# Performance work log

Hardware: AMD Instinct MI355X
Metric: run time of the kernel (lower is better)

## Reference

```python
import jax, jax.numpy as jnp
import numpy as np

N_NODES = 50000
E = 800000
D = 64
H = 128


def _ln(x, g, b, eps=1e-5):
    m = x.mean(-1, keepdims=True)
    v = ((x - m) ** 2).mean(-1, keepdims=True)
    return (x - m) * jax.lax.rsqrt(v + eps) * g + b


def setup_inputs() -> dict:
    key = jax.random.key(0)
    ks = jax.random.split(key, 8)
    return dict(
        node_emb=jax.random.normal(ks[0], (N_NODES, D), jnp.float32),
        src=jax.random.randint(ks[1], (E,), 0, N_NODES),
        dst=jax.random.randint(ks[2], (E,), 0, N_NODES),
        noise=jax.random.uniform(ks[3], (E,), jnp.float32, 1e-6, 1.0 - 1e-6),
        W1=jax.random.normal(ks[4], (2 * D, H), jnp.float32) * 0.05,
        b1=jnp.zeros((H,), jnp.float32),
        g1=jnp.ones((H,), jnp.float32),
        bt1=jnp.zeros((H,), jnp.float32),
        W2=jax.random.normal(ks[5], (H, H // 2), jnp.float32) * 0.05,
        b2=jnp.zeros((H // 2,), jnp.float32),
        g2=jnp.ones((H // 2,), jnp.float32),
        bt2=jnp.zeros((H // 2,), jnp.float32),
        W3=jax.random.normal(ks[6], (H // 2, 1), jnp.float32) * 0.05,
        b3=jnp.zeros((1,), jnp.float32),
    )


def reference(node_emb, src, dst, noise, W1, b1, g1, bt1, W2, b2, g2, bt2, W3, b3):
    # edge gather + concat: [E, 2D]
    edge_emb = jnp.concatenate([node_emb[src], node_emb[dst]], axis=1)
    # edge MLP with LayerNorm + relu (dropout=0 / eval)
    h = jax.nn.relu(_ln(edge_emb @ W1 + b1, g1, bt1))
    h = jax.nn.relu(_ln(h @ W2 + b2, g2, bt2))
    logit = (h @ W3 + b3).reshape(-1)  # [E]
    # concrete gate, bias=0, beta=1.0 (forward default)
    beta = 1.0
    gate = jax.nn.sigmoid((jnp.log(noise) - jnp.log1p(-noise) + logit) / beta)
    # degree norm: out_deg(src)^-1/2 * in_deg(dst)^-1/2, degrees clamped to >=1
    ones = jnp.ones((src.shape[0],), node_emb.dtype)
    out_deg = jnp.maximum(jax.ops.segment_sum(ones, src, num_segments=N_NODES), 1.0)
    in_deg = jnp.maximum(jax.ops.segment_sum(ones, dst, num_segments=N_NODES), 1.0)
    norm = jax.lax.rsqrt(out_deg)[src] * jax.lax.rsqrt(in_deg)[dst]
    return gate * norm
```

## Files before the change

kernel.cpp:

```cpp
#include <hip/hip_runtime.h>
#include <hip/hip_bf16.h>

#define N_NODES 50000
#define NE      800000
#define NT32    (NE / 32)
#define NTILES  (NE / 16)

typedef __attribute__((ext_vector_type(8)))  short bf16x8;
typedef __attribute__((ext_vector_type(4)))  float f32x4;
typedef __attribute__((ext_vector_type(16))) float f32x16;
typedef __attribute__((ext_vector_type(4)))  int   i32x4;
typedef __attribute__((ext_vector_type(2)))  int   i32x2;

static __device__ __forceinline__ short f2bf(float x) {
    union { float f; unsigned u; } v; v.f = x;
    unsigned r = (v.u + 0x7fffu + ((v.u >> 16) & 1u)) >> 16;
    return (short)r;
}
static __device__ __forceinline__ float bflo(unsigned u) {
    union { unsigned u; float f; } v; v.u = u << 16; return v.f;
}
static __device__ __forceinline__ float bfhi(unsigned u) {
    union { unsigned u; float f; } v; v.u = u & 0xffff0000u; return v.f;
}
static __device__ __forceinline__ float bfs(unsigned short u) {
    union { unsigned u; float f; } v; v.u = ((unsigned)u) << 16; return v.f;
}
static __device__ __forceinline__ unsigned pk2bf(float a, float b) {
    union { __hip_bfloat162 h; unsigned u; } v;
    float2 f; f.x = a; f.y = b;
    v.h = __float22bfloat162_rn(f);
    return v.u;
}

#define OFF_W2   32768
#define OFF_B1   49152
#define OFF_B2   49408
#define OFF_GT1  49536
#define OFF_GT2  50048
#define OFF_W3   50304
#define IMG_B    50432
#define IMG_V4   (IMG_B / 16)


__global__ void prep_hist(const float* __restrict__ emb,
                          const int* __restrict__ src, const int* __restrict__ dst,
                          const float* __restrict__ W1, const float* __restrict__ b1,
                          const float* __restrict__ g1, const float* __restrict__ bt1,
                          const float* __restrict__ W2, const float* __restrict__ b2,
                          const float* __restrict__ g2, const float* __restrict__ bt2,
                          const float* __restrict__ W3,
                          ushort* __restrict__ embB, char* __restrict__ img,
                          int* __restrict__ outd, int* __restrict__ ind)
{
    const int i0 = blockIdx.x * 256 + threadIdx.x;
    const int n  = gridDim.x * 256;

    for (int t = i0; t < (N_NODES * 64 / 8); t += n) {
        const f32x4* p = (const f32x4*)(emb + (size_t)t * 8);
        f32x4 a = p[0], b = p[1];
        unsigned u0 = pk2bf(a[0], a[1]);
        unsigned u1 = pk2bf(a[2], a[3]);
        unsigned u2 = pk2bf(b[0], b[1]);
        unsigned u3 = pk2bf(b[2], b[3]);
        i32x4 o = {(int)u0, (int)u1, (int)u2, (int)u3};
        *(i32x4*)(embB + (size_t)t * 8) = o;
    }
    for (int t = i0; t < NE; t += n) {
        atomicAdd(outd + src[t], 1);
        atomicAdd(ind + dst[t], 1);
    }
    ushort* W1f = (ushort*)img;
    for (int t = i0; t < 16384; t += n) {
        int j = t & 7, lane = (t >> 3) & 63, f = t >> 9;
        int mt = f >> 3, ke = f & 7, h = lane >> 5, c = lane & 31;
        W1f[t] = f2bf(W1[(16 * ke + 8 * h + j) * 128 + 32 * mt + c]);
    }
    ushort* W2f = (ushort*)(img + OFF_W2);
    for (int t = i0; t < 8192; t += n) {
        int j = t & 7, lane = (t >> 3) & 63, f = t >> 9;
        int mt = f >> 3, ke = f & 7, h = lane >> 5, c = lane & 31;
        W2f[t] = f2bf(W2[(16 * ke + 8 * h + j) * 64 + 32 * mt + c]);
    }
    if (i0 < 128) ((ushort*)(img + OFF_B1))[i0] = f2bf(b1[i0]);
    if (i0 < 64)  ((ushort*)(img + OFF_B2))[i0] = f2bf(b2[i0]);
    if (i0 < 128) {
        int r4 = i0 & 3, h = (i0 >> 2) & 1, q4 = (i0 >> 3) & 3, mt = i0 >> 5;
        int f = 32 * mt + 8 * q4 + 4 * h + r4;
        ((unsigned*)(img + OFF_GT1))[i0] =
            (unsigned)(ushort)f2bf(g1[f]) | ((unsigned)(ushort)f2bf(bt1[f]) << 16);
    }
    if (i0 < 64) {
        int r4 = i0 & 3, h = (i0 >> 2) & 1, q4 = (i0 >> 3) & 3, mt = i0 >> 5;
        int f = 32 * mt + 8 * q4 + 4 * h + r4;
        ((unsigned*)(img + OFF_GT2))[i0] =
            (unsigned)(ushort)f2bf(g2[f]) | ((unsigned)(ushort)f2bf(bt2[f]) << 16);
        ((ushort*)(img + OFF_W3))[i0] = f2bf(W3[f]);
    }
}


__global__ __launch_bounds__(256, 3) void edge_mlp32(
    const ushort* __restrict__ embB,
    const int*   __restrict__ src, const int* __restrict__ dst,
    const float* __restrict__ noise,
    const i32x4* __restrict__ WFimg,
    const float* __restrict__ b3p,
    const int* __restrict__ outd, const int* __restrict__ ind,
    float* __restrict__ out)
{
    __shared__ i32x4 ldsv[IMG_V4];
    char* ldsb = (char*)ldsv;

    const int tid = threadIdx.x;
    for (int i = tid; i < IMG_V4; i += 256) ldsv[i] = WFimg[i];
    __syncthreads();

    const int wid = tid >> 6;
    const int l   = tid & 63;
    const int h   = l >> 5;
    const int c   = l & 31;

    const float b3v = b3p[0];

    bf16x8 bone = {};
    bone[0] = (h == 0) ? (short)0x3F80 : (short)0;

    const int gw = blockIdx.x * 4 + wid;
    const int nw = gridDim.x * 4;

    int sn, dn;
    bf16x8 fA0, fA1, fA2, fA3, fB0, fB1, fB2, fB3;
    {
        int t0 = (gw < NT32) ? gw : (NT32 - 1);
        int e0p = t0 * 32 + c;
        sn = src[e0p]; dn = dst[e0p];
        const ushort* sp = embB + (size_t)sn * 64;
        const ushort* dp = embB + (size_t)dn * 64;
        fA0 = *(const bf16x8*)(sp + 8 * h);
        fA1 = *(const bf16x8*)(sp + 16 + 8 * h);
        fA2 = *(const bf16x8*)(sp + 32 + 8 * h);
        fA3 = *(const bf16x8*)(sp + 48 + 8 * h);
        fB0 = *(const bf16x8*)(dp + 8 * h);
        fB1 = *(const bf16x8*)(dp + 16 + 8 * h);
        fB2 = *(const bf16x8*)(dp + 32 + 8 * h);
        fB3 = *(const bf16x8*)(dp + 48 + 8 * h);
    }

    for (int tile = gw; tile < NT32; tile += nw) {
        unsigned tz;
        asm volatile("v_mov_b32 %0, 0" : "=v"(tz));
        const char* ldz = ldsb + tz;

        const int e0 = tile * 32 + c;

        const int tn  = tile + nw;
        const int tcl = (tn < NT32) ? tn : tile;
        const int e0n = tcl * 32 + c;
        int snN = src[e0n];
        int dnN = dst[e0n];
        float nz = noise[e0];
        int odv = outd[sn];
        int idv = ind[dn];

        const ushort* W1z = (const ushort*)ldz;
        f32x16 acc[4] = {};
        {
            bf16x8 bfr[8] = {fA0, fA1, fA2, fA3, fB0, fB1, fB2, fB3};
#pragma unroll
            for (int ke = 0; ke < 8; ++ke) {
#pragma unroll
                for (int mt = 0; mt < 4; ++mt) {
                    bf16x8 w = *(const bf16x8*)(W1z + (mt * 8 + ke) * 512 + l * 8);
                    acc[mt] = __builtin_amdgcn_mfma_f32_32x32x16_bf16(w, bfr[ke], acc[mt], 0, 0, 0);
                }
            }
        }
        const ushort* b1z = (const ushort*)(ldz + OFF_B1);
#pragma unroll
        for (int mt = 0; mt < 4; ++mt) {
            bf16x8 w = {};
            short bv = b1z[32 * mt + c];
            w[0] = (h == 0) ? bv : (short)0;
            acc[mt] = __builtin_amdgcn_mfma_f32_32x32x16_bf16(w, bone, acc[mt], 0, 0, 0);
        }

        float s0 = 0.f, s1 = 0.f, q0 = 0.f, q1 = 0.f;
#pragma unroll
        for (int mt = 0; mt < 4; ++mt) {
#pragma unroll
            for (int i = 0; i < 16; i += 2) {
                float v0 = acc[mt][i], v1 = acc[mt][i + 1];
                s0 += v0; q0 = fmaf(v0, v0, q0);
                s1 += v1; q1 = fmaf(v1, v1, q1);
            }
        }
        float s = s0 + s1, q = q0 + q1;
        s += __shfl_xor(s, 32);
        q += __shfl_xor(q, 32);
        const float mu = s * (1.0f / 128.0f);
        const float rs = rsqrtf(q * (1.0f / 128.0f) - mu * mu + 1e-5f);
        const float c0 = -mu * rs;

        const ushort* W2z = (const ushort*)(ldz + OFF_W2);
        f32x16 acc2[2] = {};
#pragma unroll
        for (int mt = 0; mt < 4; ++mt) {
            unsigned pk[4][2];
#pragma unroll
            for (int q4 = 0; q4 < 4; ++q4) {
                i32x4 pg = *(const i32x4*)(ldz + OFF_GT1 + ((mt * 4 + q4) * 2 + h) * 16);
                float t[4];
#pragma unroll
                for (int r4 = 0; r4 < 4; ++r4) {
                    unsigned u = (unsigned)pg[r4];
                    float v = acc[mt][q4 * 4 + r4];
                    float w = fmaf(v, rs, c0);
                    float y = fmaf(w, bflo(u), bfhi(u));
                    t[r4] = fmaxf(y, 0.f);
                }
                pk[q4][0] = pk2bf(t[0], t[1]);
                pk[q4][1] = pk2bf(t[2], t[3]);
            }
#pragma unroll
            for (int sub = 0; sub < 2; ++sub) {
                const int ke = 2 * mt + sub;
                const int qa = 2 * sub, qb = qa + 1;
                unsigned S0 = h ? pk[qa][0] : pk[qb][0];
                unsigned S1 = h ? pk[qa][1] : pk[qb][1];
                unsigned r0 = (unsigned)__shfl_xor((int)S0, 32);
                unsigned r1 = (unsigned)__shfl_xor((int)S1, 32);
                unsigned o0 = h ? pk[qb][0] : pk[qa][0];
                unsigned o1 = h ? pk[qb][1] : pk[qa][1];
                union { i32x4 i; bf16x8 b; } u;
                u.i[0] = (int)(h ? r0 : o0);
                u.i[1] = (int)(h ? r1 : o1);
                u.i[2] = (int)(h ? o0 : r0);
                u.i[3] = (int)(h ? o1 : r1);
#pragma unroll
                for (int mt2 = 0; mt2 < 2; ++mt2) {
                    bf16x8 w = *(const bf16x8*)(W2z + (mt2 * 8 + ke) * 512 + l * 8);
                    acc2[mt2] = __builtin_amdgcn_mfma_f32_32x32x16_bf16(w, u.b, acc2[mt2], 0, 0, 0);
                }
            }
        }
        const ushort* b2z = (const ushort*)(ldz + OFF_B2);
#pragma unroll
        for (int mt2 = 0; mt2 < 2; ++mt2) {
            bf16x8 w = {};
            short bv = b2z[32 * mt2 + c];
            w[0] = (h == 0) ? bv : (short)0;
            acc2[mt2] = __builtin_amdgcn_mfma_f32_32x32x16_bf16(w, bone, acc2[mt2], 0, 0, 0);
        }

        {
            const ushort* spn = embB + (size_t)snN * 64;
            const ushort* dpn = embB + (size_t)dnN * 64;
            fA0 = *(const bf16x8*)(spn + 8 * h);
            fA1 = *(const bf16x8*)(spn + 16 + 8 * h);
            fA2 = *(const bf16x8*)(spn + 32 + 8 * h);
            fA3 = *(const bf16x8*)(spn + 48 + 8 * h);
            fB0 = *(const bf16x8*)(dpn + 8 * h);
            fB1 = *(const bf16x8*)(dpn + 16 + 8 * h);
            fB2 = *(const bf16x8*)(dpn + 32 + 8 * h);
            fB3 = *(const bf16x8*)(dpn + 48 + 8 * h);
        }

        float t0 = 0.f, t1 = 0.f, p0 = 0.f, p1 = 0.f;
#pragma unroll
        for (int mt2 = 0; mt2 < 2; ++mt2) {
#pragma unroll
            for (int i = 0; i < 16; i += 2) {
                float v0 = acc2[mt2][i], v1 = acc2[mt2][i + 1];
                t0 += v0; p0 = fmaf(v0, v0, p0);
                t1 += v1; p1 = fmaf(v1, v1, p1);
            }
        }
        float s2 = t0 + t1, q2 = p0 + p1;
        s2 += __shfl_xor(s2, 32);
        q2 += __shfl_xor(q2, 32);
        const float mu2 = s2 * (1.0f / 64.0f);
        const float rs2 = rsqrtf(q2 * (1.0f / 64.0f) - mu2 * mu2 + 1e-5f);
        const float c02 = -mu2 * rs2;

        float lg = 0.f;
#pragma unroll
        for (int mt2 = 0; mt2 < 2; ++mt2) {
#pragma unroll
            for (int q4 = 0; q4 < 4; ++q4) {
                const int bse = (mt2 * 4 + q4) * 2 + h;
                i32x4 pg = *(const i32x4*)(ldz + OFF_GT2 + bse * 16);
                i32x2 wq = *(const i32x2*)(ldz + OFF_W3 + bse * 8);
#pragma unroll
                for (int r4 = 0; r4 < 4; ++r4) {
                    unsigned ug = (unsigned)pg[r4];
                    unsigned short uw = (unsigned short)(((unsigned)wq[r4 >> 1]) >> (16 * (r4 & 1)));
                    float v = acc2[mt2][q4 * 4 + r4];
                    float w = fmaf(v, rs2, c02);
                    float y = fmaf(w, bflo(ug), bfhi(ug));
                    y = fmaxf(y, 0.f);
                    lg = fmaf(y, bfs(uw), lg);
                }
            }
        }
        lg += __shfl_xor(lg, 32);
        lg += b3v;

        if (h == 0) {
            float z = __logf(nz) - log1pf(-nz) + lg;
            float gate = 1.0f / (1.0f + __expf(-z));
            int od = odv; if (od < 1) od = 1;
            int idg = idv; if (idg < 1) idg = 1;
            out[e0] = gate * (rsqrtf((float)od) * rsqrtf((float)idg));
        }

        sn = snN; dn = dnN;
    }
}


__global__ void degree_hist(const int* __restrict__ src, const int* __restrict__ dst,
                            int* __restrict__ outd, int* __restrict__ ind) {
    int i = blockIdx.x * 256 + threadIdx.x;
    if (i < NE) {
        atomicAdd(outd + src[i], 1);
        atomicAdd(ind + dst[i], 1);
    }
}

__global__ __launch_bounds__(256, 2) void edge_mlp_mfma(
    const float* __restrict__ emb,
    const int*   __restrict__ src, const int* __restrict__ dst,
    const float* __restrict__ noise,
    const float* __restrict__ W1, const float* __restrict__ b1,
    const float* __restrict__ g1, const float* __restrict__ bt1,
    const float* __restrict__ W2, const float* __restrict__ b2,
    const float* __restrict__ g2, const float* __restrict__ bt2,
    const float* __restrict__ W3, const float* __restrict__ b3,
    const int*   __restrict__ outd, const int* __restrict__ ind,
    float* __restrict__ out)
{
    __shared__ short lds[32768];
    const int tid = threadIdx.x;
    const int wid = tid >> 6;
    const int l   = tid & 63;
    const int g   = l >> 4;
    const int c   = l & 15;

    for (int i = tid; i < 16384; i += 256) {
        int j = i & 7, lane = (i >> 3) & 63, p = i >> 9;
        int ks = p >> 3, t = p & 7;
        int row = ks * 32 + (lane >> 4) * 8 + j;
        int col = t * 16 + (lane & 15);
        lds[i] = f2bf(W1[row * 128 + col]);
    }
    for (int i = tid; i < 8192; i += 256) {
        int j = i & 7, lane = (i >> 3) & 63, p = i >> 9;
        int ks = p >> 2, t = p & 3;
        int row = ks * 32 + (lane >> 4) * 8 + j;
        int col = t * 16 + (lane & 15);
        lds[16384 + i] = f2bf(W2[row * 64 + col]);
    }
    __syncthreads();

    short* Hl = lds + 24576 + wid * 2048;
    float b1v[8], g1v[8], t1v[8];
#pragma unroll
    for (int t = 0; t < 8; ++t) { int f = t * 16 + c; b1v[t] = b1[f]; g1v[t] = g1[f]; t1v[t] = bt1[f]; }
    float b2v[4], g2v[4], t2v[4], w3v[4];
#pragma unroll
    for (int t = 0; t < 4; ++t) { int f = t * 16 + c; b2v[t] = b2[f]; g2v[t] = g2[f]; t2v[t] = bt2[f]; w3v[t] = W3[f]; }
    const float b3v = b3[0];

    const int gw = blockIdx.x * 4 + wid;
    const int nw = gridDim.x * 4;

    for (int tile = gw; tile < NTILES; tile += nw) {
        const int e0 = tile * 16 + c;
        const int sn = src[e0], dn = dst[e0];
        const f32x4* sp = (const f32x4*)(emb + (size_t)sn * 64);
        const f32x4* dp = (const f32x4*)(emb + (size_t)dn * 64);
        f32x4 u[8];
        u[0] = sp[2 * g]; u[1] = sp[2 * g + 1];
        u[2] = sp[8 + 2 * g]; u[3] = sp[8 + 2 * g + 1];
        u[4] = dp[2 * g]; u[5] = dp[2 * g + 1];
        u[6] = dp[8 + 2 * g]; u[7] = dp[8 + 2 * g + 1];

        bf16x8 a1[4];
#pragma unroll
        for (int ks = 0; ks < 4; ++ks) {
            f32x4 x0 = u[2 * ks], x1 = u[2 * ks + 1];
            bf16x8 a;
            a[0] = f2bf(x0[0]); a[1] = f2bf(x0[1]); a[2] = f2bf(x0[2]); a[3] = f2bf(x0[3]);
            a[4] = f2bf(x1[0]); a[5] = f2bf(x1[1]); a[6] = f2bf(x1[2]); a[7] = f2bf(x1[3]);
            a1[ks] = a;
        }
        f32x4 acc1[8];
#pragma unroll
        for (int t = 0; t < 8; ++t) { f32x4 z = {b1v[t], b1v[t], b1v[t], b1v[t]}; acc1[t] = z; }
#pragma unroll
        for (int ks = 0; ks < 4; ++ks) {
#pragma unroll
            for (int t = 0; t < 8; ++t) {
                bf16x8 b = *(const bf16x8*)(lds + (ks * 8 + t) * 512 + l * 8);
                acc1[t] = __builtin_amdgcn_mfma_f32_16x16x32_bf16(a1[ks], b, acc1[t], 0, 0, 0);
            }
        }
        float mean[4], rstd[4];
#pragma unroll
        for (int r = 0; r < 4; ++r) {
            float s = acc1[0][r];
#pragma unroll
            for (int t = 1; t < 8; ++t) s += acc1[t][r];
            s += __shfl_xor(s, 1); s += __shfl_xor(s, 2);
            s += __shfl_xor(s, 4); s += __shfl_xor(s, 8);
            float m = s * (1.0f / 128.0f);
            float q = 0.f;
#pragma unroll
            for (int t = 0; t < 8; ++t) { float d = acc1[t][r] - m; q = fmaf(d, d, q); }
            q += __shfl_xor(q, 1); q += __shfl_xor(q, 2);
            q += __shfl_xor(q, 4); q += __shfl_xor(q, 8);
            mean[r] = m; rstd[r] = rsqrtf(q * (1.0f / 128.0f) + 1e-5f);
        }
#pragma unroll
        for (int r = 0; r < 4; ++r) {
            int rw = g * 4 + r;
            int swz = (rw & 7) << 3;
#pragma unroll
            for (int t = 0; t < 8; ++t) {
                float y = fmaf((acc1[t][r] - mean[r]) * rstd[r], g1v[t], t1v[t]);
                y = fmaxf(y, 0.f);
                Hl[rw * 128 + ((t * 16 + c) ^ swz)] = f2bf(y);
            }
        }
        bf16x8 a2[4];
        const int swzr = (c & 7) << 3;
#pragma unroll
        for (int ks = 0; ks < 4; ++ks)
            a2[ks] = *(const bf16x8*)(Hl + c * 128 + ((ks * 32 + g * 8) ^ swzr));

        f32x4 acc2[4];
#pragma unroll
        for (int t = 0; t < 4; ++t) { f32x4 z = {b2v[t], b2v[t], b2v[t], b2v[t]}; acc2[t] = z; }
#pragma unroll
        for (int ks = 0; ks < 4; ++ks) {
#pragma unroll
            for (int t = 0; t < 4; ++t) {
                bf16x8 b = *(const bf16x8*)(lds + 16384 + (ks * 4 + t) * 512 + l * 8);
                acc2[t] = __builtin_amdgcn_mfma_f32_16x16x32_bf16(a2[ks], b, acc2[t], 0, 0, 0);
            }
        }
        float logit[4];
#pragma unroll
        for (int r = 0; r < 4; ++r) {
            float s = acc2[0][r] + acc2[1][r] + acc2[2][r] + acc2[3][r];
            s += __shfl_xor(s, 1); s += __shfl_xor(s, 2);
            s += __shfl_xor(s, 4); s += __shfl_xor(s, 8);
            float m = s * (1.0f / 64.0f);
            float q = 0.f;
#pragma unroll
            for (int t = 0; t < 4; ++t) { float d = acc2[t][r] - m; q = fmaf(d, d, q); }
            q += __shfl_xor(q, 1); q += __shfl_xor(q, 2);
            q += __shfl_xor(q, 4); q += __shfl_xor(q, 8);
            float rs = rsqrtf(q * (1.0f / 64.0f) + 1e-5f);
            float p = 0.f;
#pragma unroll
            for (int t = 0; t < 4; ++t) {
                float y = fmaf((acc2[t][r] - m) * rs, g2v[t], t2v[t]);
                y = fmaxf(y, 0.f);
                p = fmaf(y, w3v[t], p);
            }
            p += __shfl_xor(p, 1); p += __shfl_xor(p, 2);
            p += __shfl_xor(p, 4); p += __shfl_xor(p, 8);
            logit[r] = p + b3v;
        }
        if (c < 4) {
            int e = tile * 16 + g * 4 + c;
            float lg = (c == 0) ? logit[0] : (c == 1) ? logit[1] : (c == 2) ? logit[2] : logit[3];
            float nz = noise[e];
            float z = __logf(nz) - log1pf(-nz) + lg;
            float gate = 1.0f / (1.0f + __expf(-z));
            int od = outd[src[e]]; if (od < 1) od = 1;
            int idg = ind[dst[e]]; if (idg < 1) idg = 1;
            out[e] = gate * (rsqrtf((float)od) * rsqrtf((float)idg));
        }
    }
}


extern "C" void kernel_launch(void* const* d_in, const int* in_sizes, int n_in,
                              void* d_out, int out_size, void* d_ws, size_t ws_size,
                              hipStream_t stream) {
    const float* emb   = (const float*)d_in[0];
    const int*   src   = (const int*)  d_in[1];
    const int*   dst   = (const int*)  d_in[2];
    const float* noise = (const float*)d_in[3];
    const float* W1  = (const float*)d_in[4];
    const float* b1  = (const float*)d_in[5];
    const float* g1  = (const float*)d_in[6];
    const float* bt1 = (const float*)d_in[7];
    const float* W2  = (const float*)d_in[8];
    const float* b2  = (const float*)d_in[9];
    const float* g2  = (const float*)d_in[10];
    const float* bt2 = (const float*)d_in[11];
    const float* W3  = (const float*)d_in[12];
    const float* b3  = (const float*)d_in[13];

    char* ws = (char*)d_ws;
    const size_t NEED = 6400000 + IMG_B + 400000;

    if (ws_size >= NEED) {
        ushort* embB = (ushort*)ws;
        char*   img  = ws + 6400000;
        int* outd = (int*)(ws + 6400000 + IMG_B);
        int* ind  = outd + N_NODES;

        hipMemsetAsync(outd, 0, 2 * N_NODES * sizeof(int), stream);
        prep_hist<<<2048, 256, 0, stream>>>(emb, src, dst, W1, b1, g1, bt1,
                                            W2, b2, g2, bt2, W3,
                                            embB, img, outd, ind);
        edge_mlp32<<<768, 256, 0, stream>>>(embB, src, dst, noise, (const i32x4*)img,
                                            b3, outd, ind, (float*)d_out);
    } else {
        int* outd = (int*)ws;
        int* ind  = outd + N_NODES;
        hipMemsetAsync(outd, 0, 2 * N_NODES * sizeof(int), stream);
        degree_hist<<<(NE + 255) / 256, 256, 0, stream>>>(src, dst, outd, ind);
        edge_mlp_mfma<<<512, 256, 0, stream>>>(emb, src, dst, noise,
                                               W1, b1, g1, bt1,
                                               W2, b2, g2, bt2,
                                               W3, b3, outd, ind,
                                               (float*)d_out);
    }
}
```

Measured before the change: 156.0 us.

## Switch edge MLP to 16x16x32 MFMA tiles with 16-edge wave tiles

Rewrites the edge MLP kernel to process 16 edges per wave using 16x16x32 bf16 MFMAs instead of 32 edges with 32x32x16. Weight images are re-laid out to match the new fragment shapes. The layer-2 operand exchange now uses ds_bpermute instead of xor shuffles, and the grid is doubled. The degree histogram also reads src/dst as int4 vectors. The aim is smaller accumulator footprint (fewer VGPRs) and more waves in flight to hide gather latency, at the cost of more per-tile overhead and extra cross-lane permutes.

```diff
diff --git a/kernel.cpp b/kernel.cpp
--- a/kernel.cpp
+++ b/kernel.cpp
@@ -3,12 +3,11 @@
 
 #define N_NODES 50000
 #define NE      800000
-#define NT32    (NE / 32)
+#define NT16    (NE / 16)
 #define NTILES  (NE / 16)
 
 typedef __attribute__((ext_vector_type(8)))  short bf16x8;
 typedef __attribute__((ext_vector_type(4)))  float f32x4;
-typedef __attribute__((ext_vector_type(16))) float f32x16;
 typedef __attribute__((ext_vector_type(4)))  int   i32x4;
 typedef __attribute__((ext_vector_type(2)))  int   i32x2;
 
@@ -22,9 +21,6 @@
 }
 static __device__ __forceinline__ float bfhi(unsigned u) {
     union { unsigned u; float f; } v; v.u = u & 0xffff0000u; return v.f;
-}
-static __device__ __forceinline__ float bfs(unsigned short u) {
-    union { unsigned u; float f; } v; v.u = ((unsigned)u) << 16; return v.f;
 }
 static __device__ __forceinline__ unsigned pk2bf(float a, float b) {
     union { __hip_bfloat162 h; unsigned u; } v;
@@ -66,41 +62,40 @@
         i32x4 o = {(int)u0, (int)u1, (int)u2, (int)u3};
         *(i32x4*)(embB + (size_t)t * 8) = o;
     }
-    for (int t = i0; t < NE; t += n) {
-        atomicAdd(outd + src[t], 1);
-        atomicAdd(ind + dst[t], 1);
+    for (int t = i0; t < NE / 4; t += n) {
+        i32x4 s4 = ((const i32x4*)src)[t];
+        i32x4 d4 = ((const i32x4*)dst)[t];
+        atomicAdd(outd + s4[0], 1); atomicAdd(outd + s4[1], 1);
+        atomicAdd(outd + s4[2], 1); atomicAdd(outd + s4[3], 1);
+        atomicAdd(ind + d4[0], 1); atomicAdd(ind + d4[1], 1);
+        atomicAdd(ind + d4[2], 1); atomicAdd(ind + d4[3], 1);
     }
     ushort* W1f = (ushort*)img;
     for (int t = i0; t < 16384; t += n) {
         int j = t & 7, lane = (t >> 3) & 63, f = t >> 9;
-        int mt = f >> 3, ke = f & 7, h = lane >> 5, c = lane & 31;
-        W1f[t] = f2bf(W1[(16 * ke + 8 * h + j) * 128 + 32 * mt + c]);
+        int tt = f >> 2, ks = f & 3, g = lane >> 4, c = lane & 15;
+        W1f[t] = f2bf(W1[(ks * 32 + g * 8 + j) * 128 + tt * 16 + c]);
     }
     ushort* W2f = (ushort*)(img + OFF_W2);
     for (int t = i0; t < 8192; t += n) {
         int j = t & 7, lane = (t >> 3) & 63, f = t >> 9;
-        int mt = f >> 3, ke = f & 7, h = lane >> 5, c = lane & 31;
-        W2f[t] = f2bf(W2[(16 * ke + 8 * h + j) * 64 + 32 * mt + c]);
+        int t2 = f >> 2, ks = f & 3, g = lane >> 4, c = lane & 15;
+        W2f[t] = f2bf(W2[(ks * 32 + g * 8 + j) * 64 + t2 * 16 + c]);
     }
     if (i0 < 128) ((ushort*)(img + OFF_B1))[i0] = f2bf(b1[i0]);
     if (i0 < 64)  ((ushort*)(img + OFF_B2))[i0] = f2bf(b2[i0]);
-    if (i0 < 128) {
-        int r4 = i0 & 3, h = (i0 >> 2) & 1, q4 = (i0 >> 3) & 3, mt = i0 >> 5;
-        int f = 32 * mt + 8 * q4 + 4 * h + r4;
+    if (i0 < 128)
         ((unsigned*)(img + OFF_GT1))[i0] =
-            (unsigned)(ushort)f2bf(g1[f]) | ((unsigned)(ushort)f2bf(bt1[f]) << 16);
-    }
+            (unsigned)(ushort)f2bf(g1[i0]) | ((unsigned)(ushort)f2bf(bt1[i0]) << 16);
     if (i0 < 64) {
-        int r4 = i0 & 3, h = (i0 >> 2) & 1, q4 = (i0 >> 3) & 3, mt = i0 >> 5;
-        int f = 32 * mt + 8 * q4 + 4 * h + r4;
         ((unsigned*)(img + OFF_GT2))[i0] =
-            (unsigned)(ushort)f2bf(g2[f]) | ((unsigned)(ushort)f2bf(bt2[f]) << 16);
-        ((ushort*)(img + OFF_W3))[i0] = f2bf(W3[f]);
-    }
-}
-
-
-__global__ __launch_bounds__(256, 3) void edge_mlp32(
+            (unsigned)(ushort)f2bf(g2[i0]) | ((unsigned)(ushort)f2bf(bt2[i0]) << 16);
+        ((ushort*)(img + OFF_W3))[i0] = f2bf(W3[i0]);
+    }
+}
+
+
+__global__ __launch_bounds__(256, 3) void edge_mlp16(
     const ushort* __restrict__ embB,
     const int*   __restrict__ src, const int* __restrict__ dst,
     const float* __restrict__ noise,
@@ -116,47 +111,45 @@
     for (int i = tid; i < IMG_V4; i += 256) ldsv[i] = WFimg[i];
     __syncthreads();
 
-    const int wid = tid >> 6;
-    const int l   = tid & 63;
-    const int h   = l >> 5;
-    const int c   = l & 31;
+    const int l = tid & 63;
+    const int g = l >> 4;
+    const int c = l & 15;
 
     const float b3v = b3p[0];
 
     bf16x8 bone = {};
-    bone[0] = (h == 0) ? (short)0x3F80 : (short)0;
-
-    const int gw = blockIdx.x * 4 + wid;
+    bone[0] = (g == 0) ? (short)0x3F80 : (short)0;
+
+    const int addrA = (((g & 1) * 2) * 16 + c) * 4;
+    const int addrB = addrA + 64;
+
+    const int gw = blockIdx.x * 4 + (tid >> 6);
     const int nw = gridDim.x * 4;
 
     int sn, dn;
-    bf16x8 fA0, fA1, fA2, fA3, fB0, fB1, fB2, fB3;
+    bf16x8 fS0, fS1, fD0, fD1;
     {
-        int t0 = (gw < NT32) ? gw : (NT32 - 1);
-        int e0p = t0 * 32 + c;
+        int t0 = (gw < NT16) ? gw : (NT16 - 1);
+        int e0p = t0 * 16 + c;
         sn = src[e0p]; dn = dst[e0p];
         const ushort* sp = embB + (size_t)sn * 64;
         const ushort* dp = embB + (size_t)dn * 64;
-        fA0 = *(const bf16x8*)(sp + 8 * h);
-        fA1 = *(const bf16x8*)(sp + 16 + 8 * h);
-        fA2 = *(const bf16x8*)(sp + 32 + 8 * h);
-        fA3 = *(const bf16x8*)(sp + 48 + 8 * h);
-        fB0 = *(const bf16x8*)(dp + 8 * h);
-        fB1 = *(const bf16x8*)(dp + 16 + 8 * h);
-        fB2 = *(const bf16x8*)(dp + 32 + 8 * h);
-        fB3 = *(const bf16x8*)(dp + 48 + 8 * h);
-    }
-
-    for (int tile = gw; tile < NT32; tile += nw) {
+        fS0 = *(const bf16x8*)(sp + g * 8);
+        fS1 = *(const bf16x8*)(sp + 32 + g * 8);
+        fD0 = *(const bf16x8*)(dp + g * 8);
+        fD1 = *(const bf16x8*)(dp + 32 + g * 8);
+    }
+
+    for (int tile = gw; tile < NT16; tile += nw) {
         unsigned tz;
         asm volatile("v_mov_b32 %0, 0" : "=v"(tz));
         const char* ldz = ldsb + tz;
 
-        const int e0 = tile * 32 + c;
+        const int e0 = tile * 16 + c;
 
         const int tn  = tile + nw;
-        const int tcl = (tn < NT32) ? tn : tile;
-        const int e0n = tcl * 32 + c;
+        const int tcl = (tn < NT16) ? tn : tile;
+        const int e0n = tcl * 16 + c;
         int snN = src[e0n];
         int dnN = dst[e0n];
         float nz = noise[e0];
@@ -164,149 +157,133 @@
         int idv = ind[dn];
 
         const ushort* W1z = (const ushort*)ldz;
-        f32x16 acc[4] = {};
-        {
-            bf16x8 bfr[8] = {fA0, fA1, fA2, fA3, fB0, fB1, fB2, fB3};
-#pragma unroll
-            for (int ke = 0; ke < 8; ++ke) {
-#pragma unroll
-                for (int mt = 0; mt < 4; ++mt) {
-                    bf16x8 w = *(const bf16x8*)(W1z + (mt * 8 + ke) * 512 + l * 8);
-                    acc[mt] = __builtin_amdgcn_mfma_f32_32x32x16_bf16(w, bfr[ke], acc[mt], 0, 0, 0);
-                }
+        f32x4 acc1[8] = {};
+#pragma unroll
+        for (int ks = 0; ks < 4; ++ks) {
+            bf16x8 bf = (ks == 0) ? fS0 : (ks == 1) ? fS1 : (ks == 2) ? fD0 : fD1;
+#pragma unroll
+            for (int t = 0; t < 8; ++t) {
+                bf16x8 w = *(const bf16x8*)(W1z + (t * 4 + ks) * 512 + l * 8);
+                acc1[t] = __builtin_amdgcn_mfma_f32_16x16x32_bf16(w, bf, acc1[t], 0, 0, 0);
             }
         }
         const ushort* b1z = (const ushort*)(ldz + OFF_B1);
 #pragma unroll
-        for (int mt = 0; mt < 4; ++mt) {
+        for (int t = 0; t < 8; ++t) {
             bf16x8 w = {};
-            short bv = b1z[32 * mt + c];
-            w[0] = (h == 0) ? bv : (short)0;
-            acc[mt] = __builtin_amdgcn_mfma_f32_32x32x16_bf16(w, bone, acc[mt], 0, 0, 0);
+            short bv = b1z[t * 16 + c];
+            w[0] = (g == 0) ? bv : (short)0;
+            acc1[t] = __builtin_amdgcn_mfma_f32_16x16x32_bf16(w, bone, acc1[t], 0, 0, 0);
         }
 
         float s0 = 0.f, s1 = 0.f, q0 = 0.f, q1 = 0.f;
 #pragma unroll
-        for (int mt = 0; mt < 4; ++mt) {
-#pragma unroll
-            for (int i = 0; i < 16; i += 2) {
-                float v0 = acc[mt][i], v1 = acc[mt][i + 1];
-                s0 += v0; q0 = fmaf(v0, v0, q0);
-                s1 += v1; q1 = fmaf(v1, v1, q1);
-            }
+        for (int t = 0; t < 8; ++t) {
+            float v0 = acc1[t][0], v1 = acc1[t][1], v2 = acc1[t][2], v3 = acc1[t][3];
+            s0 += v0 + v2; q0 = fmaf(v0, v0, fmaf(v2, v2, q0));
+            s1 += v1 + v3; q1 = fmaf(v1, v1, fmaf(v3, v3, q1));
         }
         float s = s0 + s1, q = q0 + q1;
-        s += __shfl_xor(s, 32);
-        q += __shfl_xor(q, 32);
+        s += __shfl_xor(s, 16); s += __shfl_xor(s, 32);
+        q += __shfl_xor(q, 16); q += __shfl_xor(q, 32);
         const float mu = s * (1.0f / 128.0f);
         const float rs = rsqrtf(q * (1.0f / 128.0f) - mu * mu + 1e-5f);
         const float c0 = -mu * rs;
 
+        unsigned pku[8][2];
+#pragma unroll
+        for (int t = 0; t < 8; ++t) {
+            i32x4 pg = *(const i32x4*)(ldz + OFF_GT1 + t * 64 + g * 16);
+            float y0, y1, y2, y3;
+            {
+                float w0 = fmaf(acc1[t][0], rs, c0);
+                y0 = fmaxf(fmaf(w0, bflo((unsigned)pg[0]), bfhi((unsigned)pg[0])), 0.f);
+                float w1 = fmaf(acc1[t][1], rs, c0);
+                y1 = fmaxf(fmaf(w1, bflo((unsigned)pg[1]), bfhi((unsigned)pg[1])), 0.f);
+                float w2 = fmaf(acc1[t][2], rs, c0);
+                y2 = fmaxf(fmaf(w2, bflo((unsigned)pg[2]), bfhi((unsigned)pg[2])), 0.f);
+                float w3 = fmaf(acc1[t][3], rs, c0);
+                y3 = fmaxf(fmaf(w3, bflo((unsigned)pg[3]), bfhi((unsigned)pg[3])), 0.f);
+            }
+            pku[t][0] = pk2bf(y0, y1);
+            pku[t][1] = pk2bf(y2, y3);
+        }
+
         const ushort* W2z = (const ushort*)(ldz + OFF_W2);
-        f32x16 acc2[2] = {};
-#pragma unroll
-        for (int mt = 0; mt < 4; ++mt) {
-            unsigned pk[4][2];
-#pragma unroll
-            for (int q4 = 0; q4 < 4; ++q4) {
-                i32x4 pg = *(const i32x4*)(ldz + OFF_GT1 + ((mt * 4 + q4) * 2 + h) * 16);
-                float t[4];
-#pragma unroll
-                for (int r4 = 0; r4 < 4; ++r4) {
-                    unsigned u = (unsigned)pg[r4];
-                    float v = acc[mt][q4 * 4 + r4];
-                    float w = fmaf(v, rs, c0);
-                    float y = fmaf(w, bflo(u), bfhi(u));
-                    t[r4] = fmaxf(y, 0.f);
-                }
-                pk[q4][0] = pk2bf(t[0], t[1]);
-                pk[q4][1] = pk2bf(t[2], t[3]);
-            }
-#pragma unroll
-            for (int sub = 0; sub < 2; ++sub) {
-                const int ke = 2 * mt + sub;
-                const int qa = 2 * sub, qb = qa + 1;
-                unsigned S0 = h ? pk[qa][0] : pk[qb][0];
-                unsigned S1 = h ? pk[qa][1] : pk[qb][1];
-                unsigned r0 = (unsigned)__shfl_xor((int)S0, 32);
-                unsigned r1 = (unsigned)__shfl_xor((int)S1, 32);
-                unsigned o0 = h ? pk[qb][0] : pk[qa][0];
-                unsigned o1 = h ? pk[qb][1] : pk[qa][1];
-                union { i32x4 i; bf16x8 b; } u;
-                u.i[0] = (int)(h ? r0 : o0);
-                u.i[1] = (int)(h ? r1 : o1);
-                u.i[2] = (int)(h ? o0 : r0);
-                u.i[3] = (int)(h ? o1 : r1);
-#pragma unroll
-                for (int mt2 = 0; mt2 < 2; ++mt2) {
-                    bf16x8 w = *(const bf16x8*)(W2z + (mt2 * 8 + ke) * 512 + l * 8);
-                    acc2[mt2] = __builtin_amdgcn_mfma_f32_32x32x16_bf16(w, u.b, acc2[mt2], 0, 0, 0);
-                }
+        f32x4 acc2[4] = {};
+#pragma unroll
+        for (int ks = 0; ks < 4; ++ks) {
+            int a0 = __builtin_amdgcn_ds_bpermute(addrA, (int)pku[2 * ks][0]);
+            int b0 = __builtin_amdgcn_ds_bpermute(addrA, (int)pku[2 * ks + 1][0]);
+            int a1 = __builtin_amdgcn_ds_bpermute(addrA, (int)pku[2 * ks][1]);
+            int b1_ = __builtin_amdgcn_ds_bpermute(addrA, (int)pku[2 * ks + 1][1]);
+            int a2 = __builtin_amdgcn_ds_bpermute(addrB, (int)pku[2 * ks][0]);
+            int b2_ = __builtin_amdgcn_ds_bpermute(addrB, (int)pku[2 * ks + 1][0]);
+            int a3 = __builtin_amdgcn_ds_bpermute(addrB, (int)pku[2 * ks][1]);
+            int b3_ = __builtin_amdgcn_ds_bpermute(addrB, (int)pku[2 * ks + 1][1]);
+            union { i32x4 i; bf16x8 b; } u;
+            u.i[0] = (g & 2) ? b0 : a0;
+            u.i[1] = (g & 2) ? b1_ : a1;
+            u.i[2] = (g & 2) ? b2_ : a2;
+            u.i[3] = (g & 2) ? b3_ : a3;
+#pragma unroll
+            for (int t2 = 0; t2 < 4; ++t2) {
+                bf16x8 w = *(const bf16x8*)(W2z + (t2 * 4 + ks) * 512 + l * 8);
+                acc2[t2] = __builtin_amdgcn_mfma_f32_16x16x32_bf16(w, u.b, acc2[t2], 0, 0, 0);
             }
         }
         const ushort* b2z = (const ushort*)(ldz + OFF_B2);
 #pragma unroll
-        for (int mt2 = 0; mt2 < 2; ++mt2) {
+        for (int t2 = 0; t2 < 4; ++t2) {
             bf16x8 w = {};
-            short bv = b2z[32 * mt2 + c];
-            w[0] = (h == 0) ? bv : (short)0;
-            acc2[mt2] = __builtin_amdgcn_mfma_f32_32x32x16_bf16(w, bone, acc2[mt2], 0, 0, 0);
+            short bv = b2z[t2 * 16 + c];
+            w[0] = (g == 0) ? bv : (short)0;
+            acc2[t2] = __builtin_amdgcn_mfma_f32_16x16x32_bf16(w, bone, acc2[t2], 0, 0, 0);
         }
 
         {
             const ushort* spn = embB + (size_t)snN * 64;
             const ushort* dpn = embB + (size_t)dnN * 64;
-            fA0 = *(const bf16x8*)(spn + 8 * h);
-            fA1 = *(const bf16x8*)(spn + 16 + 8 * h);
-            fA2 = *(const bf16x8*)(spn + 32 + 8 * h);
-            fA3 = *(const bf16x8*)(spn + 48 + 8 * h);
-            fB0 = *(const bf16x8*)(dpn + 8 * h);
-            fB1 = *(const bf16x8*)(dpn + 16 + 8 * h);
-            fB2 = *(const bf16x8*)(dpn + 32 + 8 * h);
-            fB3 = *(const bf16x8*)(dpn + 48 + 8 * h);
+            fS0 = *(const bf16x8*)(spn + g * 8);
+            fS1 = *(const bf16x8*)(spn + 32 + g * 8);
+            fD0 = *(const bf16x8*)(dpn + g * 8);
+            fD1 = *(const bf16x8*)(dpn + 32 + g * 8);
         }
 
         float t0 = 0.f, t1 = 0.f, p0 = 0.f, p1 = 0.f;
 #pragma unroll
-        for (int mt2 = 0; mt2 < 2; ++mt2) {
-#pragma unroll
-            for (int i = 0; i < 16; i += 2) {
-                float v0 = acc2[mt2][i], v1 = acc2[mt2][i + 1];
-                t0 += v0; p0 = fmaf(v0, v0, p0);
-                t1 += v1; p1 = fmaf(v1, v1, p1);
-            }
+        for (int t2 = 0; t2 < 4; ++t2) {
+            float v0 = acc2[t2][0], v1 = acc2[t2][1], v2 = acc2[t2][2], v3 = acc2[t2][3];
+            t0 += v0 + v2; p0 = fmaf(v0, v0, fmaf(v2, v2, p0));
+            t1 += v1 + v3; p1 = fmaf(v1, v1, fmaf(v3, v3, p1));
         }
         float s2 = t0 + t1, q2 = p0 + p1;
-        s2 += __shfl_xor(s2, 32);
-        q2 += __shfl_xor(q2, 32);
+        s2 += __shfl_xor(s2, 16); s2 += __shfl_xor(s2, 32);
+        q2 += __shfl_xor(q2, 16); q2 += __shfl_xor(q2, 32);
         const float mu2 = s2 * (1.0f / 64.0f);
         const float rs2 = rsqrtf(q2 * (1.0f / 64.0f) - mu2 * mu2 + 1e-5f);
         const float c02 = -mu2 * rs2;
 
         float lg = 0.f;
 #pragma unroll
-        for (int mt2 = 0; mt2 < 2; ++mt2) {
-#pragma unroll
-            for (int q4 = 0; q4 < 4; ++q4) {
-                const int bse = (mt2 * 4 + q4) * 2 + h;
-                i32x4 pg = *(const i32x4*)(ldz + OFF_GT2 + bse * 16);
-                i32x2 wq = *(const i32x2*)(ldz + OFF_W3 + bse * 8);
-#pragma unroll
-                for (int r4 = 0; r4 < 4; ++r4) {
-                    unsigned ug = (unsigned)pg[r4];
-                    unsigned short uw = (unsigned short)(((unsigned)wq[r4 >> 1]) >> (16 * (r4 & 1)));
-                    float v = acc2[mt2][q4 * 4 + r4];
-                    float w = fmaf(v, rs2, c02);
-                    float y = fmaf(w, bflo(ug), bfhi(ug));
-                    y = fmaxf(y, 0.f);
-                    lg = fmaf(y, bfs(uw), lg);
-                }
-            }
-        }
+        for (int t2 = 0; t2 < 4; ++t2) {
+            i32x4 pg = *(const i32x4*)(ldz + OFF_GT2 + t2 * 64 + g * 16);
+            i32x2 wq = *(const i32x2*)(ldz + OFF_W3 + t2 * 32 + g * 8);
+#pragma unroll
+            for (int r = 0; r < 4; ++r) {
+                unsigned ug = (unsigned)pg[r];
+                unsigned wu = (unsigned)wq[r >> 1];
+                float w3v = (r & 1) ? bfhi(wu) : bflo(wu);
+                float w = fmaf(acc2[t2][r], rs2, c02);
+                float y = fmaxf(fmaf(w, bflo(ug), bfhi(ug)), 0.f);
+                lg = fmaf(y, w3v, lg);
+            }
+        }
+        lg += __shfl_xor(lg, 16);
         lg += __shfl_xor(lg, 32);
         lg += b3v;
 
-        if (h == 0) {
+        if (g == 0) {
             float z = __logf(nz) - log1pf(-nz) + lg;
             float gate = 1.0f / (1.0f + __expf(-z));
             int od = odv; if (od < 1) od = 1;
@@ -519,8 +496,8 @@
         prep_hist<<<2048, 256, 0, stream>>>(emb, src, dst, W1, b1, g1, bt1,
                                             W2, b2, g2, bt2, W3,
                                             embB, img, outd, ind);
-        edge_mlp32<<<768, 256, 0, stream>>>(embB, src, dst, noise, (const i32x4*)img,
-                                            b3, outd, ind, (float*)d_out);
+        edge_mlp16<<<1536, 256, 0, stream>>>(embB, src, dst, noise, (const i32x4*)img,
+                                             b3, outd, ind, (float*)d_out);
     } else {
         int* outd = (int*)ws;
         int* ind  = outd + N_NODES;
```

Result: slower. 172.2 us (+10.3%).
